# Kernel tuning notes

Hardware: AMD Instinct MI355X
Metric: run time of the kernel (lower is better)

Reference implementation:

```python
import jax, jax.numpy as jnp
import numpy as np


def setup_inputs() -> dict:
    key = jax.random.key(0)
    ks = jax.random.split(key, 5)
    B, S, D, L = 16, 256, 768, 32
    return {
        "head": jax.random.normal(ks[0], (B, S, D), dtype=jnp.float32),
        "dep": jax.random.normal(ks[1], (B, S, D), dtype=jnp.float32),
        "label_U_diag": jax.random.normal(ks[2], (L, D), dtype=jnp.float32) * 0.02,
        "label_W": jax.random.normal(ks[3], (L, 2 * D), dtype=jnp.float32) * 0.02,
        "label_b": jax.random.normal(ks[4], (L,), dtype=jnp.float32) * 0.02,
    }


def reference(head, dep, label_U_diag, label_W, label_b):
    # head, dep: [b, s, d]; label_U_diag: [l, d]; label_W: [l, 2d]; label_b: [l]
    d = head.shape[-1]
    # Bilinear term with diagonal U: t1[b,l,i,o] = sum_d head[b,i,d]*U[l,d]*dep[b,o,d]
    t1 = jnp.einsum('bid,ld,bod->blio', head, label_U_diag, dep)
    # Linear term: W @ concat(head_i, dep_o) = W_h @ head_i + W_d @ dep_o
    W_h, W_d = label_W[:, :d], label_W[:, d:]
    t2_h = jnp.einsum('ld,bid->bli', W_h, head)  # [b, l, s]
    t2_d = jnp.einsum('ld,bod->blo', W_d, dep)   # [b, l, s]
    return t1 + t2_h[:, :, :, None] + t2_d[:, :, None, :] + label_b[None, :, None, None]
```

## Files before the change

### kernel.cpp

```cpp
#include <hip/hip_runtime.h>
#include <hip/hip_bf16.h>
#include <stdint.h>


#define B_ 16
#define S_ 256
#define D_ 768
#define L_ 32

typedef unsigned short ushort_t;
typedef __attribute__((ext_vector_type(4))) float f32x4;
typedef __attribute__((ext_vector_type(8))) short s16x8;

typedef __attribute__((address_space(1))) const unsigned int guint;
typedef __attribute__((address_space(3))) unsigned int luint;

__device__ __forceinline__ void async_load16(const ushort_t* g, ushort_t* l) {
  __builtin_amdgcn_global_load_lds((guint*)g, (luint*)l, 16, 0, 0);
}

__device__ __forceinline__ unsigned int pack_bf16(float f0, float f1) {
  unsigned int u0 = __builtin_bit_cast(unsigned int, f0) + 0x8000u;
  unsigned int u1 = __builtin_bit_cast(unsigned int, f1) + 0x8000u;
  return __builtin_amdgcn_perm(u1, u0, 0x07060302);
}

__global__ __launch_bounds__(256) void prep_kernel(
    const float* __restrict__ head, const float* __restrict__ dep,
    const float* __restrict__ labelW,
    ushort_t* __restrict__ depb,
    float* __restrict__ t2h, float* __restrict__ t2d) {
  __shared__ float Ss[64][64];
  __shared__ float Ws[32][65];

  const int z = blockIdx.x;
  const int ic = z & 3;
  const int sel = (z >> 2) & 1;
  const int b = z >> 3;
  const int i0 = ic * 64;
  const float* src = sel ? dep : head;
  float* t2x = sel ? t2d : t2h;
  const int t = threadIdx.x;

  const int ig = t >> 3;
  const int lg = t & 7;
  float acc[2][4] = {{0.f, 0.f, 0.f, 0.f}, {0.f, 0.f, 0.f, 0.f}};

  const int srow = t >> 2;
  const int sd0 = (t & 3) * 16;

  for (int dc = 0; dc < D_; dc += 64) {
    __syncthreads();
    {
      const int wl = t >> 3, wd0 = (t & 7) * 8;
      const float* wp = labelW + (size_t)wl * (2 * D_) + sel * D_ + dc + wd0;
#pragma unroll
      for (int j = 0; j < 8; ++j) Ws[wl][wd0 + j] = wp[j];
    }
    {
      const float* sp = src + ((size_t)(b * S_ + i0 + srow)) * D_ + dc + sd0;
      float4 v0 = *(const float4*)(sp);
      float4 v1 = *(const float4*)(sp + 4);
      float4 v2 = *(const float4*)(sp + 8);
      float4 v3 = *(const float4*)(sp + 12);
      float arr[16] = {v0.x, v0.y, v0.z, v0.w, v1.x, v1.y, v1.z, v1.w,
                       v2.x, v2.y, v2.z, v2.w, v3.x, v3.y, v3.z, v3.w};
#pragma unroll
      for (int j = 0; j < 16; ++j) Ss[sd0 + j][srow] = arr[j];
      if (sel) {
        unsigned int pk[8];
#pragma unroll
        for (int j = 0; j < 8; ++j) pk[j] = pack_bf16(arr[2 * j], arr[2 * j + 1]);
        unsigned int* dp =
            (unsigned int*)(depb + ((size_t)(b * S_ + i0 + srow)) * D_ + dc + sd0);
        uint4 w0 = {pk[0], pk[1], pk[2], pk[3]};
        uint4 w1 = {pk[4], pk[5], pk[6], pk[7]};
        *(uint4*)(dp) = w0;
        *(uint4*)(dp + 4) = w1;
      }
    }
    __syncthreads();
#pragma unroll 4
    for (int dd = 0; dd < 64; ++dd) {
      const float s0 = Ss[dd][ig * 2 + 0];
      const float s1 = Ss[dd][ig * 2 + 1];
#pragma unroll
      for (int j = 0; j < 4; ++j) {
        const float w = Ws[lg * 4 + j][dd];
        acc[0][j] += s0 * w;
        acc[1][j] += s1 * w;
      }
    }
  }
#pragma unroll
  for (int j = 0; j < 4; ++j) {
    const int l = lg * 4 + j;
    float* op = t2x + ((size_t)(b * L_ + l)) * S_ + i0 + ig * 2;
    op[0] = acc[0][j];
    op[1] = acc[1][j];
  }
}

__global__ __launch_bounds__(256) void main_kernel(
    const float* __restrict__ head, const ushort_t* __restrict__ depb,
    const float* __restrict__ U, const float* __restrict__ bias,
    const float* __restrict__ t2h, const float* __restrict__ t2d,
    float* __restrict__ out) {
  __shared__ ushort_t As[128 * 32];
  __shared__ ushort_t Bs[128 * 32];
  __shared__ float Us[D_];
  __shared__ float T2[256];

  const int bid = blockIdx.x;
  const int tile = bid & 3;
  const int bl = bid >> 2;
  const int l = bl & (L_ - 1);
  const int b = bl >> 5;
  const int ti = (tile >> 1) * 128;
  const int to = (tile & 1) * 128;
  const int t = threadIdx.x;
  const int lane = t & 63;
  const int wave = t >> 6;
  const int m_base = (wave >> 1) * 64;
  const int n_base = (wave & 1) * 64;

  for (int i = t; i < D_ / 4; i += 256)
    ((float4*)Us)[i] = ((const float4*)(U + (size_t)l * D_))[i];
  if (t < 128)
    T2[t] = t2h[((size_t)(b * L_ + l)) * S_ + ti + t];
  else
    T2[t] = t2d[((size_t)(b * L_ + l)) * S_ + to + (t - 128)];
  const float bv = bias[l];

  const int row0 = t >> 2;
  const int kq = (t & 3) * 8;
  const float* hp0 = head + ((size_t)(b * S_ + ti + row0)) * D_ + kq;
  const float* hp1 = hp0 + (size_t)64 * D_;
  const ushort_t* dp0 = depb + ((size_t)(b * S_ + to + row0)) * D_ + kq;
  const ushort_t* dp1 = dp0 + (size_t)64 * D_;
  ushort_t* asw0 = As + t * 8;
  ushort_t* asw1 = As + (256 + t) * 8;
  ushort_t* bsw0 = Bs + t * 8;
  ushort_t* bsw1 = Bs + (256 + t) * 8;

  f32x4 acc[4][4];
#pragma unroll
  for (int i = 0; i < 4; ++i)
#pragma unroll
    for (int j = 0; j < 4; ++j) acc[i][j] = {0.f, 0.f, 0.f, 0.f};

  const ushort_t* ar = As + ((m_base + (lane & 15)) * 32 + (lane >> 4) * 8);
  const ushort_t* br = Bs + ((n_base + (lane & 15)) * 32 + (lane >> 4) * 8);

  for (int kk = 0; kk < D_; kk += 32) {
    __syncthreads();
    async_load16(dp0 + kk, bsw0);
    async_load16(dp1 + kk, bsw1);
    float4 h0 = *(const float4*)(hp0 + kk);
    float4 h1 = *(const float4*)(hp0 + kk + 4);
    float4 h2 = *(const float4*)(hp1 + kk);
    float4 h3 = *(const float4*)(hp1 + kk + 4);
    float4 u0 = *(const float4*)(Us + kk + kq);
    float4 u1 = *(const float4*)(Us + kk + kq + 4);
    uint4 w0, w1;
    w0.x = pack_bf16(h0.x * u0.x, h0.y * u0.y);
    w0.y = pack_bf16(h0.z * u0.z, h0.w * u0.w);
    w0.z = pack_bf16(h1.x * u1.x, h1.y * u1.y);
    w0.w = pack_bf16(h1.z * u1.z, h1.w * u1.w);
    w1.x = pack_bf16(h2.x * u0.x, h2.y * u0.y);
    w1.y = pack_bf16(h2.z * u0.z, h2.w * u0.w);
    w1.z = pack_bf16(h3.x * u1.x, h3.y * u1.y);
    w1.w = pack_bf16(h3.z * u1.z, h3.w * u1.w);
    *(uint4*)asw0 = w0;
    *(uint4*)asw1 = w1;
    __syncthreads();

    s16x8 af[4], bf[4];
#pragma unroll
    for (int rt = 0; rt < 4; ++rt) af[rt] = *(const s16x8*)(ar + rt * 16 * 32);
#pragma unroll
    for (int ct = 0; ct < 4; ++ct) bf[ct] = *(const s16x8*)(br + ct * 16 * 32);
#pragma unroll
    for (int rt = 0; rt < 4; ++rt)
#pragma unroll
      for (int ct = 0; ct < 4; ++ct)
        acc[rt][ct] = __builtin_amdgcn_mfma_f32_16x16x32_bf16(af[rt], bf[ct],
                                                              acc[rt][ct], 0, 0, 0);
  }

  const int colg = lane & 15;
  const int rgrp = lane >> 4;
  float* ob = out + (((size_t)(b * L_ + l)) * S_ + ti) * S_ + to;
#pragma unroll
  for (int rt = 0; rt < 4; ++rt) {
    const int r0 = m_base + rt * 16 + rgrp * 4;
#pragma unroll
    for (int ct = 0; ct < 4; ++ct) {
      const int c = n_base + ct * 16 + colg;
      const float addc = T2[128 + c] + bv;
      float* p = ob + (size_t)r0 * S_ + c;
#pragma unroll
      for (int r = 0; r < 4; ++r)
        p[(size_t)r * S_] = acc[rt][ct][r] + T2[r0 + r] + addc;
    }
  }
}

extern "C" void kernel_launch(void* const* d_in, const int* in_sizes, int n_in,
                              void* d_out, int out_size, void* d_ws, size_t ws_size,
                              hipStream_t stream) {
  const float* head = (const float*)d_in[0];
  const float* dep = (const float*)d_in[1];
  const float* U = (const float*)d_in[2];
  const float* W = (const float*)d_in[3];
  const float* bias = (const float*)d_in[4];
  float* out = (float*)d_out;

  ushort_t* depb = (ushort_t*)d_ws;
  float* t2h = (float*)((char*)d_ws + (size_t)B_ * S_ * D_ * 2);
  float* t2d = t2h + (size_t)B_ * L_ * S_;

  prep_kernel<<<B_ * 2 * 4, 256, 0, stream>>>(head, dep, W, depb, t2h, t2d);
  main_kernel<<<B_ * L_ * 4, 256, 0, stream>>>(head, depb, U, bias, t2h, t2d, out);
}
```

Before: 255.5 us.

## Rewrite prep as wave-per-row-group reduction and widen main tile to 128x256

The prep kernel now gives each wave four rows and reduces the 32 label dot products with cross-lane shuffles instead of LDS-tiled accumulation. This uses many more blocks (512 vs 128) to raise parallelism. The main kernel now covers a 128x256 output tile per block, so the head*U A-tile is built once per row block instead of twice, and U is read straight from global memory rather than staged in LDS. In exchange the accumulator count doubles, which raises register pressure (launch bounds now request 2 blocks per CU), and the grid halves to 1024 blocks.

```diff
diff --git a/kernel.cpp b/kernel.cpp
--- a/kernel.cpp
+++ b/kernel.cpp
@@ -27,141 +27,125 @@
 
 __global__ __launch_bounds__(256) void prep_kernel(
     const float* __restrict__ head, const float* __restrict__ dep,
-    const float* __restrict__ labelW,
-    ushort_t* __restrict__ depb,
+    const float* __restrict__ labelW, ushort_t* __restrict__ depb,
     float* __restrict__ t2h, float* __restrict__ t2d) {
-  __shared__ float Ss[64][64];
-  __shared__ float Ws[32][65];
-
-  const int z = blockIdx.x;
-  const int ic = z & 3;
-  const int sel = (z >> 2) & 1;
-  const int b = z >> 3;
-  const int i0 = ic * 64;
+  const int wave = threadIdx.x >> 6;
+  const int lane = threadIdx.x & 63;
+  const int g = blockIdx.x * 4 + wave;
+  const int sel = g >> 10;
+  const int idx = g & 1023;
+  const int b = idx >> 6;
+  const int row0 = (idx & 63) * 4;
   const float* src = sel ? dep : head;
   float* t2x = sel ? t2d : t2h;
-  const int t = threadIdx.x;
-
-  const int ig = t >> 3;
-  const int lg = t & 7;
-  float acc[2][4] = {{0.f, 0.f, 0.f, 0.f}, {0.f, 0.f, 0.f, 0.f}};
-
-  const int srow = t >> 2;
-  const int sd0 = (t & 3) * 16;
-
-  for (int dc = 0; dc < D_; dc += 64) {
-    __syncthreads();
-    {
-      const int wl = t >> 3, wd0 = (t & 7) * 8;
-      const float* wp = labelW + (size_t)wl * (2 * D_) + sel * D_ + dc + wd0;
-#pragma unroll
-      for (int j = 0; j < 8; ++j) Ws[wl][wd0 + j] = wp[j];
-    }
-    {
-      const float* sp = src + ((size_t)(b * S_ + i0 + srow)) * D_ + dc + sd0;
-      float4 v0 = *(const float4*)(sp);
-      float4 v1 = *(const float4*)(sp + 4);
-      float4 v2 = *(const float4*)(sp + 8);
-      float4 v3 = *(const float4*)(sp + 12);
-      float arr[16] = {v0.x, v0.y, v0.z, v0.w, v1.x, v1.y, v1.z, v1.w,
-                       v2.x, v2.y, v2.z, v2.w, v3.x, v3.y, v3.z, v3.w};
-#pragma unroll
-      for (int j = 0; j < 16; ++j) Ss[sd0 + j][srow] = arr[j];
-      if (sel) {
-        unsigned int pk[8];
-#pragma unroll
-        for (int j = 0; j < 8; ++j) pk[j] = pack_bf16(arr[2 * j], arr[2 * j + 1]);
-        unsigned int* dp =
-            (unsigned int*)(depb + ((size_t)(b * S_ + i0 + srow)) * D_ + dc + sd0);
-        uint4 w0 = {pk[0], pk[1], pk[2], pk[3]};
-        uint4 w1 = {pk[4], pk[5], pk[6], pk[7]};
-        *(uint4*)(dp) = w0;
-        *(uint4*)(dp + 4) = w1;
-      }
-    }
-    __syncthreads();
-#pragma unroll 4
-    for (int dd = 0; dd < 64; ++dd) {
-      const float s0 = Ss[dd][ig * 2 + 0];
-      const float s1 = Ss[dd][ig * 2 + 1];
-#pragma unroll
-      for (int j = 0; j < 4; ++j) {
-        const float w = Ws[lg * 4 + j][dd];
-        acc[0][j] += s0 * w;
-        acc[1][j] += s1 * w;
-      }
-    }
-  }
-#pragma unroll
-  for (int j = 0; j < 4; ++j) {
-    const int l = lg * 4 + j;
-    float* op = t2x + ((size_t)(b * L_ + l)) * S_ + i0 + ig * 2;
-    op[0] = acc[0][j];
-    op[1] = acc[1][j];
-  }
-}
-
-__global__ __launch_bounds__(256) void main_kernel(
+  const int d0 = lane * 12;
+
+  float h[4][12];
+  const float* rp = src + ((size_t)(b * S_ + row0)) * D_ + d0;
+#pragma unroll
+  for (int r = 0; r < 4; ++r) {
+    float4 v0 = *(const float4*)(rp + (size_t)r * D_);
+    float4 v1 = *(const float4*)(rp + (size_t)r * D_ + 4);
+    float4 v2 = *(const float4*)(rp + (size_t)r * D_ + 8);
+    h[r][0] = v0.x; h[r][1] = v0.y; h[r][2] = v0.z; h[r][3] = v0.w;
+    h[r][4] = v1.x; h[r][5] = v1.y; h[r][6] = v1.z; h[r][7] = v1.w;
+    h[r][8] = v2.x; h[r][9] = v2.y; h[r][10] = v2.z; h[r][11] = v2.w;
+  }
+  if (sel) {
+#pragma unroll
+    for (int r = 0; r < 4; ++r) {
+      uint2 q0 = {pack_bf16(h[r][0], h[r][1]), pack_bf16(h[r][2], h[r][3])};
+      uint2 q1 = {pack_bf16(h[r][4], h[r][5]), pack_bf16(h[r][6], h[r][7])};
+      uint2 q2 = {pack_bf16(h[r][8], h[r][9]), pack_bf16(h[r][10], h[r][11])};
+      uint2* dp = (uint2*)(depb + ((size_t)(b * S_ + row0 + r)) * D_ + d0);
+      dp[0] = q0; dp[1] = q1; dp[2] = q2;
+    }
+  }
+  const float* wbase = labelW + sel * D_ + d0;
+  for (int l = 0; l < L_; ++l) {
+    const float* wp = wbase + (size_t)l * (2 * D_);
+    float4 w0 = *(const float4*)(wp);
+    float4 w1 = *(const float4*)(wp + 4);
+    float4 w2 = *(const float4*)(wp + 8);
+    float w[12] = {w0.x, w0.y, w0.z, w0.w, w1.x, w1.y, w1.z, w1.w,
+                   w2.x, w2.y, w2.z, w2.w};
+    float p0 = 0.f, p1 = 0.f, p2 = 0.f, p3 = 0.f;
+#pragma unroll
+    for (int j = 0; j < 12; ++j) {
+      p0 += h[0][j] * w[j];
+      p1 += h[1][j] * w[j];
+      p2 += h[2][j] * w[j];
+      p3 += h[3][j] * w[j];
+    }
+#pragma unroll
+    for (int off = 32; off >= 1; off >>= 1) {
+      p0 += __shfl_xor(p0, off);
+      p1 += __shfl_xor(p1, off);
+      p2 += __shfl_xor(p2, off);
+      p3 += __shfl_xor(p3, off);
+    }
+    if (lane < 4) {
+      float v = lane == 0 ? p0 : lane == 1 ? p1 : lane == 2 ? p2 : p3;
+      t2x[((size_t)(b * L_ + l)) * S_ + row0 + lane] = v;
+    }
+  }
+}
+
+__global__ __launch_bounds__(256, 2) void main_kernel(
     const float* __restrict__ head, const ushort_t* __restrict__ depb,
     const float* __restrict__ U, const float* __restrict__ bias,
     const float* __restrict__ t2h, const float* __restrict__ t2d,
     float* __restrict__ out) {
   __shared__ ushort_t As[128 * 32];
-  __shared__ ushort_t Bs[128 * 32];
-  __shared__ float Us[D_];
-  __shared__ float T2[256];
+  __shared__ ushort_t Bs[256 * 32];
+  __shared__ float T2[384];
 
   const int bid = blockIdx.x;
-  const int tile = bid & 3;
-  const int bl = bid >> 2;
+  const int ic = bid & 1;
+  const int bl = bid >> 1;
   const int l = bl & (L_ - 1);
   const int b = bl >> 5;
-  const int ti = (tile >> 1) * 128;
-  const int to = (tile & 1) * 128;
+  const int ti = ic * 128;
   const int t = threadIdx.x;
   const int lane = t & 63;
   const int wave = t >> 6;
   const int m_base = (wave >> 1) * 64;
-  const int n_base = (wave & 1) * 64;
-
-  for (int i = t; i < D_ / 4; i += 256)
-    ((float4*)Us)[i] = ((const float4*)(U + (size_t)l * D_))[i];
-  if (t < 128)
-    T2[t] = t2h[((size_t)(b * L_ + l)) * S_ + ti + t];
-  else
-    T2[t] = t2d[((size_t)(b * L_ + l)) * S_ + to + (t - 128)];
+  const int n_base = (wave & 1) * 128;
+
+  for (int i = t; i < 384; i += 256)
+    T2[i] = (i < 128) ? t2h[((size_t)(b * L_ + l)) * S_ + ti + i]
+                      : t2d[((size_t)(b * L_ + l)) * S_ + (i - 128)];
   const float bv = bias[l];
 
   const int row0 = t >> 2;
   const int kq = (t & 3) * 8;
   const float* hp0 = head + ((size_t)(b * S_ + ti + row0)) * D_ + kq;
   const float* hp1 = hp0 + (size_t)64 * D_;
-  const ushort_t* dp0 = depb + ((size_t)(b * S_ + to + row0)) * D_ + kq;
-  const ushort_t* dp1 = dp0 + (size_t)64 * D_;
+  const float* Up = U + (size_t)l * D_ + kq;
+  const ushort_t* dp = depb + ((size_t)(b * S_ + row0)) * D_ + kq;
   ushort_t* asw0 = As + t * 8;
-  ushort_t* asw1 = As + (256 + t) * 8;
-  ushort_t* bsw0 = Bs + t * 8;
-  ushort_t* bsw1 = Bs + (256 + t) * 8;
-
-  f32x4 acc[4][4];
+  ushort_t* asw1 = As + t * 8 + 2048;
+
+  f32x4 acc[4][8];
 #pragma unroll
   for (int i = 0; i < 4; ++i)
 #pragma unroll
-    for (int j = 0; j < 4; ++j) acc[i][j] = {0.f, 0.f, 0.f, 0.f};
+    for (int j = 0; j < 8; ++j) acc[i][j] = {0.f, 0.f, 0.f, 0.f};
 
   const ushort_t* ar = As + ((m_base + (lane & 15)) * 32 + (lane >> 4) * 8);
   const ushort_t* br = Bs + ((n_base + (lane & 15)) * 32 + (lane >> 4) * 8);
 
   for (int kk = 0; kk < D_; kk += 32) {
     __syncthreads();
-    async_load16(dp0 + kk, bsw0);
-    async_load16(dp1 + kk, bsw1);
+#pragma unroll
+    for (int j = 0; j < 4; ++j)
+      async_load16(dp + kk + (size_t)j * 64 * D_, Bs + j * 2048 + t * 8);
     float4 h0 = *(const float4*)(hp0 + kk);
     float4 h1 = *(const float4*)(hp0 + kk + 4);
     float4 h2 = *(const float4*)(hp1 + kk);
     float4 h3 = *(const float4*)(hp1 + kk + 4);
-    float4 u0 = *(const float4*)(Us + kk + kq);
-    float4 u1 = *(const float4*)(Us + kk + kq + 4);
+    float4 u0 = *(const float4*)(Up + kk);
+    float4 u1 = *(const float4*)(Up + kk + 4);
     uint4 w0, w1;
     w0.x = pack_bf16(h0.x * u0.x, h0.y * u0.y);
     w0.y = pack_bf16(h0.z * u0.z, h0.w * u0.w);
@@ -175,27 +159,27 @@
     *(uint4*)asw1 = w1;
     __syncthreads();
 
-    s16x8 af[4], bf[4];
-#pragma unroll
-    for (int rt = 0; rt < 4; ++rt) af[rt] = *(const s16x8*)(ar + rt * 16 * 32);
-#pragma unroll
-    for (int ct = 0; ct < 4; ++ct) bf[ct] = *(const s16x8*)(br + ct * 16 * 32);
+    s16x8 af[4], bf[8];
+#pragma unroll
+    for (int rt = 0; rt < 4; ++rt) af[rt] = *(const s16x8*)(ar + rt * 512);
+#pragma unroll
+    for (int ct = 0; ct < 8; ++ct) bf[ct] = *(const s16x8*)(br + ct * 512);
 #pragma unroll
     for (int rt = 0; rt < 4; ++rt)
 #pragma unroll
-      for (int ct = 0; ct < 4; ++ct)
+      for (int ct = 0; ct < 8; ++ct)
         acc[rt][ct] = __builtin_amdgcn_mfma_f32_16x16x32_bf16(af[rt], bf[ct],
                                                               acc[rt][ct], 0, 0, 0);
   }
 
   const int colg = lane & 15;
   const int rgrp = lane >> 4;
-  float* ob = out + (((size_t)(b * L_ + l)) * S_ + ti) * S_ + to;
+  float* ob = out + (((size_t)(b * L_ + l)) * S_ + ti) * S_;
 #pragma unroll
   for (int rt = 0; rt < 4; ++rt) {
     const int r0 = m_base + rt * 16 + rgrp * 4;
 #pragma unroll
-    for (int ct = 0; ct < 4; ++ct) {
+    for (int ct = 0; ct < 8; ++ct) {
       const int c = n_base + ct * 16 + colg;
       const float addc = T2[128 + c] + bv;
       float* p = ob + (size_t)r0 * S_ + c;
@@ -220,6 +204,6 @@
   float* t2h = (float*)((char*)d_ws + (size_t)B_ * S_ * D_ * 2);
   float* t2d = t2h + (size_t)B_ * L_ * S_;
 
-  prep_kernel<<<B_ * 2 * 4, 256, 0, stream>>>(head, dep, W, depb, t2h, t2d);
-  main_kernel<<<B_ * L_ * 4, 256, 0, stream>>>(head, depb, U, bias, t2h, t2d, out);
-}
+  prep_kernel<<<512, 256, 0, stream>>>(head, dep, W, depb, t2h, t2d);
+  main_kernel<<<B_ * L_ * 2, 256, 0, stream>>>(head, depb, U, bias, t2h, t2d, out);
+}
```

After: 249.4 us. -2.4%, faster.
